# Kernel tuning notes

Hardware: AMD Instinct MI355X
Metric: run time of the kernel (lower is better)

Reference implementation:

```python
import jax, jax.numpy as jnp
import numpy as np

B, T, C, H, E, TOPK, DR = 2, 2048, 768, 3072, 8, 2, 24


def setup_inputs() -> dict:
    key = jax.random.key(0)
    ks = jax.random.split(key, 16)
    std = 0.02
    n = lambda k, shape, s=std: (s * jax.random.normal(k, shape)).astype(jnp.float32)
    emb = jax.random.normal(ks[3], (E, DR), dtype=jnp.float32)
    emb = emb / (jnp.linalg.norm(emb, axis=-1, keepdims=True) + 1e-8)
    return {
        "x": jax.random.normal(ks[0], (B, T, C), dtype=jnp.float32),
        "router_w": n(ks[1], (E, C)),
        "probe_w": n(ks[2], (DR, C)),
        "router_emb": emb,
        "fatigue": jnp.zeros((E,), jnp.float32),
        "energy": jnp.ones((E,), jnp.float32),
        "w_fast1": n(ks[4], (E, C, H)),
        "w_slow1": n(ks[5], (E, C, H)),
        "h_fast1": n(ks[6], (E, C, H), 0.005),
        "m_gate1": jax.random.uniform(ks[7], (E,), dtype=jnp.float32),
        "b1": jnp.zeros((E, H), jnp.float32),
        "w_fast2": n(ks[8], (E, H, C)),
        "w_slow2": n(ks[9], (E, H, C)),
        "h_fast2": n(ks[10], (E, H, C), 0.005),
        "m_gate2": jax.random.uniform(ks[11], (E,), dtype=jnp.float32),
        "b2": jnp.zeros((E, C), jnp.float32),
    }


def _normalize(v, axis=-1, eps=1e-12):
    # matches F.normalize: v / max(||v||, eps)
    return v / jnp.maximum(jnp.linalg.norm(v, axis=axis, keepdims=True), eps)


def reference(x, router_w, probe_w, router_emb, fatigue, energy,
              w_fast1, w_slow1, h_fast1, m_gate1, b1,
              w_fast2, w_slow2, h_fast2, m_gate2, b2):
    Bd, Td, Cd = x.shape
    # --- router logits with biology-inspired biases ---
    logits = jnp.einsum('btc,ec->bte', x, router_w)            # nn.Linear, no bias
    tok_proxy = x.mean(axis=-1, keepdims=True)                  # [B,T,1]
    router_gain = jnp.linalg.norm(router_emb, axis=-1)          # [E]
    base_bias = 0.02 * tok_proxy                                # broadcasts over E
    gain_bias = 0.02 * tok_proxy * router_gain                  # [B,T,E]
    tok_unit = _normalize(jnp.einsum('btc,dc->btd', x, probe_w))
    align_bias = 0.02 * jnp.einsum('btd,ed->bte', tok_unit, _normalize(router_emb))
    logits = logits + base_bias + gain_bias + align_bias + 0.1 * energy - 0.1 * fatigue
    # --- top-k gating ---
    g, idx = jax.lax.top_k(logits, TOPK)                        # [B,T,K]
    gates = jax.nn.softmax(g, axis=-1)
    N = Bd * Td
    gates_full = jnp.zeros((N, E), x.dtype).at[
        jnp.arange(N)[:, None], idx.reshape(N, TOPK)].set(gates.reshape(N, TOPK))
    flat_x = x.reshape(N, Cd)
    # --- expert dispatch: dynamic W = w_fast + m_gate*w_slow + H_fast ---
    def body(acc, p):
        wf1, ws1, hf1, mg1, bb1, wf2, ws2, hf2, mg2, bb2, ge = p
        W1 = wf1 + mg1 * ws1 + hf1                              # [C,H]
        h = jnp.square(jnp.maximum(flat_x @ W1 + bb1, 0.0))     # relu(y)^2
        W2 = wf2 + mg2 * ws2 + hf2                              # [H,C]
        y = h @ W2 + bb2
        return acc + ge[:, None] * y, None
    out, _ = jax.lax.scan(
        body, jnp.zeros((N, Cd), x.dtype),
        (w_fast1, w_slow1, h_fast1, m_gate1, b1,
         w_fast2, w_slow2, h_fast2, m_gate2, b2, gates_full.T))
    return out.reshape(Bd, Td, Cd)
```

## Files before the change

kernel.cpp:

```cpp
#include <hip/hip_runtime.h>

typedef unsigned short u16;
typedef __attribute__((ext_vector_type(8))) short short8;
typedef __attribute__((ext_vector_type(8))) unsigned short ushort8;
typedef __attribute__((ext_vector_type(4))) unsigned short ushort4v;
typedef __attribute__((ext_vector_type(4))) float f32x4;

static constexpr int Cdim = 768;
static constexpr int Hdim = 3072;
static constexpr int Edim = 8;
static constexpr int Ntok = 4096;
static constexpr int DRc  = 24;
static constexpr int NSLOT = Ntok * 2;
static constexpr int NCHUNK = 8;
static constexpr int CCH = Cdim / NCHUNK;

static constexpr size_t OFF_XB   = 0;
static constexpr size_t OFF_W1T  = 6291456;
static constexpr size_t OFF_W2T  = 44040192;
static constexpr size_t OFF_HBUF = 81788928;
static constexpr size_t OFF_XT   = OFF_HBUF;
static constexpr size_t OFF_PART = OFF_HBUF + 12582912;
static constexpr size_t OFF_TOK  = 132120576;
static constexpr size_t OFF_GATE = 132251648;
static constexpr size_t OFF_CNT  = 132382720;
static constexpr size_t OFF_OFFS = 132382752;

__device__ __forceinline__ u16 f2bf(float f) {
  unsigned u = __builtin_bit_cast(unsigned, f);
  u += 0x7fffu + ((u >> 16) & 1u);
  return (u16)(u >> 16);
}

__device__ __forceinline__ void gld16(const u16* g, u16* l) {
  __builtin_amdgcn_global_load_lds((const __attribute__((address_space(1))) unsigned int*)g,
                                   (__attribute__((address_space(3))) unsigned int*)l,
                                   16, 0, 0);
}

__global__ __launch_bounds__(256)
void prep_x2_kernel(const float* __restrict__ x, u16* __restrict__ x16,
                    float* __restrict__ xT) {
  __shared__ float tile[64][65];
  const int c0 = blockIdx.x * 64;
  const int t0 = blockIdx.y * 64;
  const int tid = threadIdx.x;
  const int row = tid >> 4, col = (tid & 15) * 4;
  #pragma unroll
  for (int i = 0; i < 4; i++) {
    int r = row + i * 16;
    size_t idx = (size_t)(t0 + r) * Cdim + c0 + col;
    float4 v = *(const float4*)(x + idx);
    tile[r][col + 0] = v.x; tile[r][col + 1] = v.y;
    tile[r][col + 2] = v.z; tile[r][col + 3] = v.w;
    ushort4v o = { f2bf(v.x), f2bf(v.y), f2bf(v.z), f2bf(v.w) };
    *reinterpret_cast<ushort4v*>(x16 + idx) = o;
  }
  __syncthreads();
  const int c = tid >> 2, tg = (tid & 3) * 16;
  #pragma unroll
  for (int q = 0; q < 4; q++) {
    float4 w;
    w.x = tile[tg + q * 4 + 0][c];
    w.y = tile[tg + q * 4 + 1][c];
    w.z = tile[tg + q * 4 + 2][c];
    w.w = tile[tg + q * 4 + 3][c];
    *reinterpret_cast<float4*>(xT + (size_t)(c0 + c) * Ntok + t0 + tg + q * 4) = w;
  }
}

__global__ __launch_bounds__(256)
void prep_wt_kernel(const float* __restrict__ wf, const float* __restrict__ wsl,
                    const float* __restrict__ hf, const float* __restrict__ mg,
                    u16* __restrict__ outw, const int R, const int Ccol) {
  __shared__ u16 tileT[64][66];
  const int e = blockIdx.z;
  const int r0 = blockIdx.x * 64, c0 = blockIdx.y * 64;
  const float m = mg[e];
  const size_t base = (size_t)e * R * Ccol;
  const int t = threadIdx.x;
  const int cr = t >> 4, cc = (t & 15) * 4;
  #pragma unroll
  for (int i = 0; i < 4; i++) {
    int r = cr + i * 16;
    size_t idx = base + (size_t)(r0 + r) * Ccol + (c0 + cc);
    float4 a = *(const float4*)(wf + idx);
    float4 b = *(const float4*)(wsl + idx);
    float4 h = *(const float4*)(hf + idx);
    tileT[cc + 0][r] = f2bf(fmaf(m, b.x, a.x) + h.x);
    tileT[cc + 1][r] = f2bf(fmaf(m, b.y, a.y) + h.y);
    tileT[cc + 2][r] = f2bf(fmaf(m, b.z, a.z) + h.z);
    tileT[cc + 3][r] = f2bf(fmaf(m, b.w, a.w) + h.w);
  }
  __syncthreads();
  const int oc = t >> 2, ch = (t & 3) * 16;
  ushort8 o0, o1;
  #pragma unroll
  for (int j = 0; j < 8; j++) { o0[j] = tileT[oc][ch + j]; o1[j] = tileT[oc][ch + 8 + j]; }
  size_t oidx = ((size_t)e * Ccol + c0 + oc) * R + r0 + ch;
  *reinterpret_cast<ushort8*>(outw + oidx) = o0;
  *reinterpret_cast<ushort8*>(outw + oidx + 8) = o1;
}

__global__ __launch_bounds__(256)
void logits_part_kernel(const float* __restrict__ xT, const float* __restrict__ router_w,
                        const float* __restrict__ probe_w, float* __restrict__ part) {
  const int t = blockIdx.x * 256 + threadIdx.x;
  const int cB = blockIdx.y * CCH;
  float racc[Edim] = {};
  float pacc[DRc] = {};
  float sacc = 0.f;
  for (int ci = 0; ci < CCH; ci++) {
    int c = cB + ci;
    float xv = xT[(size_t)c * Ntok + t];
    sacc += xv;
    #pragma unroll
    for (int ee = 0; ee < Edim; ee++) racc[ee] = fmaf(xv, router_w[ee * Cdim + c], racc[ee]);
    #pragma unroll
    for (int d = 0; d < DRc; d++) pacc[d] = fmaf(xv, probe_w[d * Cdim + c], pacc[d]);
  }
  float* pb = part + (size_t)blockIdx.y * 33 * Ntok + t;
  #pragma unroll
  for (int ee = 0; ee < Edim; ee++) pb[(size_t)ee * Ntok] = racc[ee];
  #pragma unroll
  for (int d = 0; d < DRc; d++) pb[(size_t)(8 + d) * Ntok] = pacc[d];
  pb[(size_t)32 * Ntok] = sacc;
}

__global__ __launch_bounds__(256)
void router_fin_kernel(const float* __restrict__ part, const float* __restrict__ emb,
                       const float* __restrict__ fatigue, const float* __restrict__ energy,
                       int* __restrict__ counts, int* __restrict__ tok_list,
                       float* __restrict__ gate_list) {
  const int t = blockIdx.x * 256 + threadIdx.x;
  float v[33];
  #pragma unroll
  for (int o = 0; o < 33; o++) {
    float s = 0.f;
    #pragma unroll
    for (int ch = 0; ch < NCHUNK; ch++)
      s += part[((size_t)ch * 33 + o) * Ntok + t];
    v[o] = s;
  }
  const float* racc = v;
  const float* pacc = v + 8;
  float proxy = v[32] / 768.f;
  float pn2 = 0.f;
  #pragma unroll
  for (int d = 0; d < DRc; d++) pn2 += pacc[d] * pacc[d];
  float pnorm = sqrtf(pn2);
  float logitv[Edim];
  #pragma unroll
  for (int ee = 0; ee < Edim; ee++) {
    float g2 = 0.f, dote = 0.f;
    #pragma unroll
    for (int d = 0; d < DRc; d++) {
      float ev = emb[ee * DRc + d];
      g2 += ev * ev;
      dote += pacc[d] * ev;
    }
    float gain = sqrtf(g2);
    float align = dote / (fmaxf(pnorm, 1e-12f) * fmaxf(gain, 1e-12f));
    logitv[ee] = racc[ee] + 0.02f * proxy * (1.f + gain) + 0.02f * align
               + 0.1f * energy[ee] - 0.1f * fatigue[ee];
  }
  int e0 = 0; float b0v = logitv[0];
  #pragma unroll
  for (int ee = 1; ee < Edim; ee++) if (logitv[ee] > b0v) { b0v = logitv[ee]; e0 = ee; }
  int e1 = -1; float b1v = -3.4e38f;
  #pragma unroll
  for (int ee = 0; ee < Edim; ee++) if (ee != e0 && logitv[ee] > b1v) { b1v = logitv[ee]; e1 = ee; }
  float texp = expf(b1v - b0v);
  float g0 = 1.f / (1.f + texp);
  float g1 = texp / (1.f + texp);
  int p0 = atomicAdd(&counts[e0], 1);
  tok_list[e0 * Ntok + p0] = t; gate_list[e0 * Ntok + p0] = g0;
  int p1 = atomicAdd(&counts[e1], 1);
  tok_list[e1 * Ntok + p1] = t; gate_list[e1 * Ntok + p1] = g1;
}

__global__ void offsets_kernel(const int* __restrict__ counts, int* __restrict__ offs) {
  if (threadIdx.x == 0) {
    int r = 0;
    for (int e = 0; e < Edim; e++) { offs[e] = r; r += counts[e]; }
  }
}

__global__ __launch_bounds__(256)
void fc1_kernel(const u16* __restrict__ x16, const u16* __restrict__ W1T,
                const float* __restrict__ b1, const int* __restrict__ counts,
                const int* __restrict__ offs, const int* __restrict__ tok_list,
                u16* __restrict__ h_buf) {
  const int e = blockIdx.z;
  const int n_e = counts[e];
  const int tokBase = blockIdx.y * 128;
  if (tokBase >= n_e) return;
  const int hBase = blockIdx.x * 128;
  __shared__ u16 As[128 * 32];
  __shared__ u16 Bs[128 * 32];
  __shared__ int toks[128];
  const int tid = threadIdx.x;
  if (tid < 128) {
    int s = tokBase + tid;
    toks[tid] = (s < n_e) ? tok_list[e * Ntok + s] : 0;
  }
  __syncthreads();
  const int lane = tid & 63, wv = tid >> 6;
  const int wr = wv >> 1, wc = wv & 1;
  const int sRow = lane >> 2, sSlot = lane & 3;
  const int kbOff = (sSlot ^ ((sRow >> 1) & 3)) * 8;
  const int rA0 = wv * 16 + sRow, rA1 = 64 + rA0;
  const u16* pA0 = x16 + (size_t)toks[rA0] * Cdim + kbOff;
  const u16* pA1 = x16 + (size_t)toks[rA1] * Cdim + kbOff;
  const u16* pB0 = W1T + ((size_t)e * Hdim + hBase + rA0) * Cdim + kbOff;
  const u16* pB1 = W1T + ((size_t)e * Hdim + hBase + rA1) * Cdim + kbOff;
  u16* ldsA0 = As + wv * 512 + lane * 8;
  u16* ldsA1 = As + 2048 + wv * 512 + lane * 8;
  u16* ldsB0 = Bs + wv * 512 + lane * 8;
  u16* ldsB1 = Bs + 2048 + wv * 512 + lane * 8;
  const int fr = lane & 15;
  const int qsw = (((lane >> 4) ^ ((fr >> 1) & 3))) * 8;
  f32x4 acc[4][4] = {};
  for (int k0 = 0; k0 < Cdim; k0 += 32) {
    gld16(pA0 + k0, ldsA0);
    gld16(pA1 + k0, ldsA1);
    gld16(pB0 + k0, ldsB0);
    gld16(pB1 + k0, ldsB1);
    __syncthreads();
    short8 aF[4], bF[4];
    #pragma unroll
    for (int m = 0; m < 4; m++)
      aF[m] = *reinterpret_cast<const short8*>(As + (wr * 64 + m * 16 + fr) * 32 + qsw);
    #pragma unroll
    for (int n = 0; n < 4; n++)
      bF[n] = *reinterpret_cast<const short8*>(Bs + (wc * 64 + n * 16 + fr) * 32 + qsw);
    #pragma unroll
    for (int m = 0; m < 4; m++)
      #pragma unroll
      for (int n = 0; n < 4; n++)
        acc[m][n] = __builtin_amdgcn_mfma_f32_16x16x32_bf16(aF[m], bF[n], acc[m][n], 0, 0, 0);
    __syncthreads();
  }
  const int rq = (lane >> 4) * 4;
  float bias[4];
  #pragma unroll
  for (int n = 0; n < 4; n++) bias[n] = b1[(size_t)e * Hdim + hBase + wc * 64 + n * 16 + fr];
  const int rowB = offs[e] + tokBase;
  #pragma unroll
  for (int m = 0; m < 4; m++) {
    #pragma unroll
    for (int j = 0; j < 4; j++) {
      int rl = wr * 64 + m * 16 + rq + j;
      if (tokBase + rl < n_e) {
        size_t rb = (size_t)(rowB + rl) * Hdim + hBase + wc * 64 + fr;
        #pragma unroll
        for (int n = 0; n < 4; n++) {
          float v = fmaxf(acc[m][n][j] + bias[n], 0.f);
          h_buf[rb + n * 16] = f2bf(v * v);
        }
      }
    }
  }
}

__global__ __launch_bounds__(256)
void fc2_kernel(const u16* __restrict__ h_buf, const u16* __restrict__ W2T,
                const float* __restrict__ b2, const int* __restrict__ counts,
                const int* __restrict__ offs, const int* __restrict__ tok_list,
                const float* __restrict__ gate_list, float* __restrict__ out) {
  const int e = blockIdx.z;
  const int n_e = counts[e];
  const int tokBase = blockIdx.y * 128;
  if (tokBase >= n_e) return;
  const int cBase = blockIdx.x * 128;
  __shared__ u16 As[128 * 32];
  __shared__ u16 Bs[128 * 32];
  __shared__ int toks[128];
  __shared__ float gts[128];
  const int tid = threadIdx.x;
  if (tid < 128) {
    int s = tokBase + tid;
    bool v = s < n_e;
    toks[tid] = v ? tok_list[e * Ntok + s] : 0;
    gts[tid]  = v ? gate_list[e * Ntok + s] : 0.f;
  }
  const int lane = tid & 63, wv = tid >> 6;
  const int wr = wv >> 1, wc = wv & 1;
  const int sRow = lane >> 2, sSlot = lane & 3;
  const int kbOff = (sSlot ^ ((sRow >> 1) & 3)) * 8;
  const int rA0 = wv * 16 + sRow, rA1 = 64 + rA0;
  const int slotB = offs[e] + tokBase;
  const int s0 = min(slotB + rA0, NSLOT - 1);
  const int s1 = min(slotB + rA1, NSLOT - 1);
  const u16* pA0 = h_buf + (size_t)s0 * Hdim + kbOff;
  const u16* pA1 = h_buf + (size_t)s1 * Hdim + kbOff;
  const u16* pB0 = W2T + ((size_t)e * Cdim + cBase + rA0) * Hdim + kbOff;
  const u16* pB1 = W2T + ((size_t)e * Cdim + cBase + rA1) * Hdim + kbOff;
  u16* ldsA0 = As + wv * 512 + lane * 8;
  u16* ldsA1 = As + 2048 + wv * 512 + lane * 8;
  u16* ldsB0 = Bs + wv * 512 + lane * 8;
  u16* ldsB1 = Bs + 2048 + wv * 512 + lane * 8;
  const int fr = lane & 15;
  const int qsw = (((lane >> 4) ^ ((fr >> 1) & 3))) * 8;
  f32x4 acc[4][4] = {};
  for (int k0 = 0; k0 < Hdim; k0 += 32) {
    gld16(pA0 + k0, ldsA0);
    gld16(pA1 + k0, ldsA1);
    gld16(pB0 + k0, ldsB0);
    gld16(pB1 + k0, ldsB1);
    __syncthreads();
    short8 aF[4], bF[4];
    #pragma unroll
    for (int m = 0; m < 4; m++)
      aF[m] = *reinterpret_cast<const short8*>(As + (wr * 64 + m * 16 + fr) * 32 + qsw);
    #pragma unroll
    for (int n = 0; n < 4; n++)
      bF[n] = *reinterpret_cast<const short8*>(Bs + (wc * 64 + n * 16 + fr) * 32 + qsw);
    #pragma unroll
    for (int m = 0; m < 4; m++)
      #pragma unroll
      for (int n = 0; n < 4; n++)
        acc[m][n] = __builtin_amdgcn_mfma_f32_16x16x32_bf16(aF[m], bF[n], acc[m][n], 0, 0, 0);
    __syncthreads();
  }
  const int rq = (lane >> 4) * 4;
  float bias[4];
  #pragma unroll
  for (int n = 0; n < 4; n++) bias[n] = b2[(size_t)e * Cdim + cBase + wc * 64 + n * 16 + fr];
  #pragma unroll
  for (int m = 0; m < 4; m++) {
    #pragma unroll
    for (int j = 0; j < 4; j++) {
      int rl = wr * 64 + m * 16 + rq + j;
      if (tokBase + rl < n_e) {
        int tok = toks[rl];
        float g = gts[rl];
        float* ob = out + (size_t)tok * Cdim + cBase + wc * 64 + fr;
        #pragma unroll
        for (int n = 0; n < 4; n++)
          atomicAdd(ob + n * 16, g * (acc[m][n][j] + bias[n]));
      }
    }
  }
}

extern "C" void kernel_launch(void* const* d_in, const int* in_sizes, int n_in,
                              void* d_out, int out_size, void* d_ws, size_t ws_size,
                              hipStream_t stream) {
  const float* x        = (const float*)d_in[0];
  const float* router_w = (const float*)d_in[1];
  const float* probe_w  = (const float*)d_in[2];
  const float* emb      = (const float*)d_in[3];
  const float* fatigue  = (const float*)d_in[4];
  const float* energy   = (const float*)d_in[5];
  const float* wf1      = (const float*)d_in[6];
  const float* ws1      = (const float*)d_in[7];
  const float* hf1      = (const float*)d_in[8];
  const float* mg1      = (const float*)d_in[9];
  const float* b1       = (const float*)d_in[10];
  const float* wf2      = (const float*)d_in[11];
  const float* ws2      = (const float*)d_in[12];
  const float* hf2      = (const float*)d_in[13];
  const float* mg2      = (const float*)d_in[14];
  const float* b2       = (const float*)d_in[15];
  float* out = (float*)d_out;
  char* ws = (char*)d_ws;

  u16*   x16       = (u16*)(ws + OFF_XB);
  u16*   W1T       = (u16*)(ws + OFF_W1T);
  u16*   W2T       = (u16*)(ws + OFF_W2T);
  u16*   hbuf      = (u16*)(ws + OFF_HBUF);
  float* xT        = (float*)(ws + OFF_XT);
  float* part      = (float*)(ws + OFF_PART);
  int*   tok_list  = (int*)(ws + OFF_TOK);
  float* gate_list = (float*)(ws + OFF_GATE);
  int*   counts    = (int*)(ws + OFF_CNT);
  int*   offs      = (int*)(ws + OFF_OFFS);

  hipMemsetAsync(counts, 0, 64, stream);
  hipMemsetAsync(out, 0, (size_t)Ntok * Cdim * sizeof(float), stream);

  prep_x2_kernel<<<dim3(Cdim / 64, Ntok / 64), 256, 0, stream>>>(x, x16, xT);
  logits_part_kernel<<<dim3(Ntok / 256, NCHUNK), 256, 0, stream>>>(xT, router_w, probe_w, part);
  router_fin_kernel<<<Ntok / 256, 256, 0, stream>>>(part, emb, fatigue, energy,
                                                    counts, tok_list, gate_list);
  prep_wt_kernel<<<dim3(Cdim / 64, Hdim / 64, Edim), 256, 0, stream>>>(wf1, ws1, hf1, mg1, W1T, Cdim, Hdim);
  prep_wt_kernel<<<dim3(Hdim / 64, Cdim / 64, Edim), 256, 0, stream>>>(wf2, ws2, hf2, mg2, W2T, Hdim, Cdim);
  offsets_kernel<<<1, 64, 0, stream>>>(counts, offs);
  fc1_kernel<<<dim3(Hdim / 128, Ntok / 128, Edim), 256, 0, stream>>>(x16, W1T, b1, counts, offs,
                                                                     tok_list, hbuf);
  fc2_kernel<<<dim3(Cdim / 128, Ntok / 128, Edim), 256, 0, stream>>>(hbuf, W2T, b2, counts, offs,
                                                                     tok_list, gate_list, out);
  (void)in_sizes; (void)n_in; (void)out_size; (void)ws_size;
}
```

Baseline: 382.2 us.

## Replace fc2 atomic scatter with per-slot output buffer and gather combine kernel

fc2 now writes un-gated expert outputs to a per-slot fp32 buffer (reusing the W1T region) instead of atomically adding gated results into the output. A new gather kernel combines each token's two expert rows with its gates, which removes the output memset and the float atomics. The fc2 token tile also shrinks from 128 to 64 rows, doubling the block count for better occupancy at the cost of more W2 reloads. The router now records per-token slot and gate info in place of the per-expert gate list.

```diff
diff --git a/kernel.cpp b/kernel.cpp
--- a/kernel.cpp
+++ b/kernel.cpp
@@ -21,15 +21,22 @@
 static constexpr size_t OFF_HBUF = 81788928;
 static constexpr size_t OFF_XT   = OFF_HBUF;
 static constexpr size_t OFF_PART = OFF_HBUF + 12582912;
+static constexpr size_t OFF_YB   = OFF_W1T;
 static constexpr size_t OFF_TOK  = 132120576;
-static constexpr size_t OFF_GATE = 132251648;
 static constexpr size_t OFF_CNT  = 132382720;
 static constexpr size_t OFF_OFFS = 132382752;
+static constexpr size_t OFF_TSLOT= 132382784;
+static constexpr size_t OFF_TG   = 132448320;
 
 __device__ __forceinline__ u16 f2bf(float f) {
   unsigned u = __builtin_bit_cast(unsigned, f);
   u += 0x7fffu + ((u >> 16) & 1u);
   return (u16)(u >> 16);
+}
+
+__device__ __forceinline__ float bf2f(u16 v) {
+  unsigned u = ((unsigned)v) << 16;
+  return __builtin_bit_cast(float, u);
 }
 
 __device__ __forceinline__ void gld16(const u16* g, u16* l) {
@@ -131,7 +138,7 @@
 void router_fin_kernel(const float* __restrict__ part, const float* __restrict__ emb,
                        const float* __restrict__ fatigue, const float* __restrict__ energy,
                        int* __restrict__ counts, int* __restrict__ tok_list,
-                       float* __restrict__ gate_list) {
+                       int4* __restrict__ tokslot, float2* __restrict__ tokgate) {
   const int t = blockIdx.x * 256 + threadIdx.x;
   float v[33];
   #pragma unroll
@@ -174,9 +181,11 @@
   float g0 = 1.f / (1.f + texp);
   float g1 = texp / (1.f + texp);
   int p0 = atomicAdd(&counts[e0], 1);
-  tok_list[e0 * Ntok + p0] = t; gate_list[e0 * Ntok + p0] = g0;
+  tok_list[e0 * Ntok + p0] = t;
   int p1 = atomicAdd(&counts[e1], 1);
-  tok_list[e1 * Ntok + p1] = t; gate_list[e1 * Ntok + p1] = g1;
+  tok_list[e1 * Ntok + p1] = t;
+  tokslot[t] = make_int4(e0, p0, e1, p1);
+  tokgate[t] = make_float2(g0, g1);
 }
 
 __global__ void offsets_kernel(const int* __restrict__ counts, int* __restrict__ offs) {
@@ -266,58 +275,45 @@
 __global__ __launch_bounds__(256)
 void fc2_kernel(const u16* __restrict__ h_buf, const u16* __restrict__ W2T,
                 const float* __restrict__ b2, const int* __restrict__ counts,
-                const int* __restrict__ offs, const int* __restrict__ tok_list,
-                const float* __restrict__ gate_list, float* __restrict__ out) {
+                const int* __restrict__ offs, float* __restrict__ ybuf) {
   const int e = blockIdx.z;
   const int n_e = counts[e];
-  const int tokBase = blockIdx.y * 128;
+  const int tokBase = blockIdx.y * 64;
   if (tokBase >= n_e) return;
   const int cBase = blockIdx.x * 128;
-  __shared__ u16 As[128 * 32];
+  __shared__ u16 As[64 * 32];
   __shared__ u16 Bs[128 * 32];
-  __shared__ int toks[128];
-  __shared__ float gts[128];
   const int tid = threadIdx.x;
-  if (tid < 128) {
-    int s = tokBase + tid;
-    bool v = s < n_e;
-    toks[tid] = v ? tok_list[e * Ntok + s] : 0;
-    gts[tid]  = v ? gate_list[e * Ntok + s] : 0.f;
-  }
   const int lane = tid & 63, wv = tid >> 6;
   const int wr = wv >> 1, wc = wv & 1;
   const int sRow = lane >> 2, sSlot = lane & 3;
   const int kbOff = (sSlot ^ ((sRow >> 1) & 3)) * 8;
-  const int rA0 = wv * 16 + sRow, rA1 = 64 + rA0;
+  const int rA = wv * 16 + sRow;
   const int slotB = offs[e] + tokBase;
-  const int s0 = min(slotB + rA0, NSLOT - 1);
-  const int s1 = min(slotB + rA1, NSLOT - 1);
-  const u16* pA0 = h_buf + (size_t)s0 * Hdim + kbOff;
-  const u16* pA1 = h_buf + (size_t)s1 * Hdim + kbOff;
-  const u16* pB0 = W2T + ((size_t)e * Cdim + cBase + rA0) * Hdim + kbOff;
-  const u16* pB1 = W2T + ((size_t)e * Cdim + cBase + rA1) * Hdim + kbOff;
-  u16* ldsA0 = As + wv * 512 + lane * 8;
-  u16* ldsA1 = As + 2048 + wv * 512 + lane * 8;
+  const int sA = min(slotB + rA, NSLOT - 1);
+  const u16* pA = h_buf + (size_t)sA * Hdim + kbOff;
+  const u16* pB0 = W2T + ((size_t)e * Cdim + cBase + rA) * Hdim + kbOff;
+  const u16* pB1 = W2T + ((size_t)e * Cdim + cBase + 64 + rA) * Hdim + kbOff;
+  u16* ldsA  = As + wv * 512 + lane * 8;
   u16* ldsB0 = Bs + wv * 512 + lane * 8;
   u16* ldsB1 = Bs + 2048 + wv * 512 + lane * 8;
   const int fr = lane & 15;
   const int qsw = (((lane >> 4) ^ ((fr >> 1) & 3))) * 8;
-  f32x4 acc[4][4] = {};
+  f32x4 acc[2][4] = {};
   for (int k0 = 0; k0 < Hdim; k0 += 32) {
-    gld16(pA0 + k0, ldsA0);
-    gld16(pA1 + k0, ldsA1);
+    gld16(pA + k0, ldsA);
     gld16(pB0 + k0, ldsB0);
     gld16(pB1 + k0, ldsB1);
     __syncthreads();
-    short8 aF[4], bF[4];
-    #pragma unroll
-    for (int m = 0; m < 4; m++)
-      aF[m] = *reinterpret_cast<const short8*>(As + (wr * 64 + m * 16 + fr) * 32 + qsw);
+    short8 aF[2], bF[4];
+    #pragma unroll
+    for (int m = 0; m < 2; m++)
+      aF[m] = *reinterpret_cast<const short8*>(As + (wr * 32 + m * 16 + fr) * 32 + qsw);
     #pragma unroll
     for (int n = 0; n < 4; n++)
       bF[n] = *reinterpret_cast<const short8*>(Bs + (wc * 64 + n * 16 + fr) * 32 + qsw);
     #pragma unroll
-    for (int m = 0; m < 4; m++)
+    for (int m = 0; m < 2; m++)
       #pragma unroll
       for (int n = 0; n < 4; n++)
         acc[m][n] = __builtin_amdgcn_mfma_f32_16x16x32_bf16(aF[m], bF[n], acc[m][n], 0, 0, 0);
@@ -326,22 +322,42 @@
   const int rq = (lane >> 4) * 4;
   float bias[4];
   #pragma unroll
-  for (int n = 0; n < 4; n++) bias[n] = b2[(size_t)e * Cdim + cBase + wc * 64 + n * 16 + fr];
-  #pragma unroll
-  for (int m = 0; m < 4; m++) {
+  for (int n = 0; n < 4; n++)
+    bias[n] = b2[(size_t)e * Cdim + cBase + wc * 64 + n * 16 + fr];
+  #pragma unroll
+  for (int m = 0; m < 2; m++) {
     #pragma unroll
     for (int j = 0; j < 4; j++) {
-      int rl = wr * 64 + m * 16 + rq + j;
+      int rl = wr * 32 + m * 16 + rq + j;
       if (tokBase + rl < n_e) {
-        int tok = toks[rl];
-        float g = gts[rl];
-        float* ob = out + (size_t)tok * Cdim + cBase + wc * 64 + fr;
+        float* ob = ybuf + (size_t)(slotB + rl) * Cdim + cBase + wc * 64 + fr;
         #pragma unroll
         for (int n = 0; n < 4; n++)
-          atomicAdd(ob + n * 16, g * (acc[m][n][j] + bias[n]));
+          ob[n * 16] = acc[m][n][j] + bias[n];
       }
     }
   }
+}
+
+__global__ __launch_bounds__(256)
+void gather_kernel(const float* __restrict__ ybuf, const int4* __restrict__ tokslot,
+                   const float2* __restrict__ tokgate, const int* __restrict__ offs,
+                   float* __restrict__ out) {
+  const int gid = blockIdx.x * 256 + threadIdx.x;
+  const int t = gid / 192;
+  const int c4 = (gid - t * 192) * 4;
+  int4 ts = tokslot[t];
+  float2 g = tokgate[t];
+  int s0 = offs[ts.x] + ts.y;
+  int s1 = offs[ts.z] + ts.w;
+  float4 y0 = *reinterpret_cast<const float4*>(ybuf + (size_t)s0 * Cdim + c4);
+  float4 y1 = *reinterpret_cast<const float4*>(ybuf + (size_t)s1 * Cdim + c4);
+  float4 o;
+  o.x = g.x * y0.x + g.y * y1.x;
+  o.y = g.x * y0.y + g.y * y1.y;
+  o.z = g.x * y0.z + g.y * y1.z;
+  o.w = g.x * y0.w + g.y * y1.w;
+  *reinterpret_cast<float4*>(out + (size_t)t * Cdim + c4) = o;
 }
 
 extern "C" void kernel_launch(void* const* d_in, const int* in_sizes, int n_in,
@@ -366,30 +382,32 @@
   float* out = (float*)d_out;
   char* ws = (char*)d_ws;
 
-  u16*   x16       = (u16*)(ws + OFF_XB);
-  u16*   W1T       = (u16*)(ws + OFF_W1T);
-  u16*   W2T       = (u16*)(ws + OFF_W2T);
-  u16*   hbuf      = (u16*)(ws + OFF_HBUF);
-  float* xT        = (float*)(ws + OFF_XT);
-  float* part      = (float*)(ws + OFF_PART);
-  int*   tok_list  = (int*)(ws + OFF_TOK);
-  float* gate_list = (float*)(ws + OFF_GATE);
-  int*   counts    = (int*)(ws + OFF_CNT);
-  int*   offs      = (int*)(ws + OFF_OFFS);
+  u16*    x16       = (u16*)(ws + OFF_XB);
+  u16*    W1T       = (u16*)(ws + OFF_W1T);
+  u16*    W2T       = (u16*)(ws + OFF_W2T);
+  u16*    hbuf      = (u16*)(ws + OFF_HBUF);
+  float*  xT        = (float*)(ws + OFF_XT);
+  float*  part      = (float*)(ws + OFF_PART);
+  float*  ybuf      = (float*)(ws + OFF_YB);
+  int*    tok_list  = (int*)(ws + OFF_TOK);
+  int*    counts    = (int*)(ws + OFF_CNT);
+  int*    offs      = (int*)(ws + OFF_OFFS);
+  int4*   tokslot   = (int4*)(ws + OFF_TSLOT);
+  float2* tokgate   = (float2*)(ws + OFF_TG);
 
   hipMemsetAsync(counts, 0, 64, stream);
-  hipMemsetAsync(out, 0, (size_t)Ntok * Cdim * sizeof(float), stream);
 
   prep_x2_kernel<<<dim3(Cdim / 64, Ntok / 64), 256, 0, stream>>>(x, x16, xT);
   logits_part_kernel<<<dim3(Ntok / 256, NCHUNK), 256, 0, stream>>>(xT, router_w, probe_w, part);
   router_fin_kernel<<<Ntok / 256, 256, 0, stream>>>(part, emb, fatigue, energy,
-                                                    counts, tok_list, gate_list);
+                                                    counts, tok_list, tokslot, tokgate);
   prep_wt_kernel<<<dim3(Cdim / 64, Hdim / 64, Edim), 256, 0, stream>>>(wf1, ws1, hf1, mg1, W1T, Cdim, Hdim);
   prep_wt_kernel<<<dim3(Hdim / 64, Cdim / 64, Edim), 256, 0, stream>>>(wf2, ws2, hf2, mg2, W2T, Hdim, Cdim);
   offsets_kernel<<<1, 64, 0, stream>>>(counts, offs);
   fc1_kernel<<<dim3(Hdim / 128, Ntok / 128, Edim), 256, 0, stream>>>(x16, W1T, b1, counts, offs,
                                                                      tok_list, hbuf);
-  fc2_kernel<<<dim3(Cdim / 128, Ntok / 128, Edim), 256, 0, stream>>>(hbuf, W2T, b2, counts, offs,
-                                                                     tok_list, gate_list, out);
+  fc2_kernel<<<dim3(Cdim / 128, Ntok / 64, Edim), 256, 0, stream>>>(hbuf, W2T, b2, counts, offs,
+                                                                    ybuf);
+  gather_kernel<<<Ntok * 192 / 256, 256, 0, stream>>>(ybuf, tokslot, tokgate, offs, out);
   (void)in_sizes; (void)n_in; (void)out_size; (void)ws_size;
 }
```

After: 406.0 us. +6.2%, slower.
